# Kernel tuning notes

Hardware: AMD Instinct MI355X
Metric: run time of the kernel (lower is better)

The kernel has to match this reference:

```python
import jax, jax.numpy as jnp
import numpy as np

B, E, S, H = 8, 1024, 2048, 16  # batch, embed_dim, seq_len, n_heads
D = E // H                       # per-head hidden dim


def setup_inputs() -> dict:
    key = jax.random.key(0)
    k1, k2 = jax.random.split(key)
    x = jax.random.normal(k1, (B, E, S), dtype=jnp.float32)
    weight = jax.random.normal(k2, (H, S), dtype=jnp.float32)  # nn.Parameter(torch.randn)
    bias = jnp.zeros((H, S), dtype=jnp.float32)                # nn.Parameter(torch.zeros)
    return {"x": x, "weight": weight, "bias": bias}


def _vector_to_matrix(v):
    # v: (H, S) -> M: (H, S, S), M[h, i, j] = v[h, j - i] if j >= i else 0
    h, m = v.shape
    i = jnp.arange(m)[:, None]
    j = jnp.arange(m)[None, :]
    off = j - i  # negative offsets wrap (same as torch fancy indexing) but are masked out
    return jnp.where(j >= i, v[:, off], jnp.zeros((), dtype=v.dtype))


def reference(x, weight, bias):
    b, e, s = x.shape
    h = weight.shape[0]
    d = e // h
    M = _vector_to_matrix(weight)  # (H, S, S)
    # Original: x.view(B,H,D,S).reshape(B*H,D,S) paired with W.repeat_interleave(B,0),
    # i.e. flat index k uses M[k // B]. Group the flat B*H axis into H contiguous
    # blocks of size B so each block shares one Toeplitz matrix (no (B*H,S,S) blowup).
    xg = x.reshape(b * h, d, s).reshape(h, b, d, s)  # block m = M[m]
    out = jnp.einsum('mbds,mst->mbdt', xg, M) + bias[:, None, None, :]
    return out.reshape(b, e, s)
```

## Files before the change

### kernel.cpp

```cpp
#include <hip/hip_runtime.h>
#include <hip/hip_bf16.h>

#define SEQ    2048
#define NHEAD  16
#define RPH    512
#define BM     128
#define BK     64
#define NTH    512

#define WSTRIDE 2184
#define ABUF_E  8192
#define WCOP_E  (2 * ABUF_E)
#define TOT_E   (WCOP_E + 8 * WSTRIDE + 128)

typedef float  f32x4  __attribute__((ext_vector_type(4)));
typedef __bf16 bf16x8 __attribute__((ext_vector_type(8)));

struct PF { float4 v0, v1, v2, v3; };

__device__ __forceinline__ unsigned f2bf(float f) {
    union { __hip_bfloat16 h; unsigned short u; } cv;
    cv.h = __float2bfloat16(f);
    return (unsigned)cv.u;
}

__device__ __forceinline__ uint4 pack8u(float4 a, float4 b) {
    union { bf16x8 v; uint4 u; } r;
    r.v[0] = (__bf16)a.x; r.v[1] = (__bf16)a.y;
    r.v[2] = (__bf16)a.z; r.v[3] = (__bf16)a.w;
    r.v[4] = (__bf16)b.x; r.v[5] = (__bf16)b.y;
    r.v[6] = (__bf16)b.z; r.v[7] = (__bf16)b.w;
    return r.u;
}

#define MFMA16(a, b, c) __builtin_amdgcn_mfma_f32_16x16x32_bf16((a), (b), (c), 0, 0, 0)

#define LOADPF(P, CH)                                                         \
  { const float* g_ = Xp + (size_t)(CH) * BK;                                 \
    P.v0 = *(const float4*)g_;                                                \
    P.v1 = *(const float4*)(g_ + 4);                                          \
    P.v2 = *(const float4*)(g_ + 8);                                          \
    P.v3 = *(const float4*)(g_ + 12); }

#define WRITEA(AB, P)                                                         \
  { *(uint4*)((AB) + wb0) = pack8u(P.v0, P.v1);                               \
    *(uint4*)((AB) + wb1) = pack8u(P.v2, P.v3); }

#define WINLOAD4(CH, OFFE, S0, S1, S2, S3)                                    \
  { const unsigned short* bq_ = wcB + 64 * (CH) + (OFFE);                     \
    bw[S0] = *(const bf16x8*)(bq_);                                           \
    bw[S1] = *(const bf16x8*)(bq_ + 16);                                      \
    bw[S2] = *(const bf16x8*)(bq_ + 32);                                      \
    bw[S3] = *(const bf16x8*)(bq_ + 48); }

#define KSTEPW(ABC, KS, P8, BASE)                                             \
  { const int kb_ = (64 * (KS) + kq16) ^ swz;                                 \
    bf16x8 af0 = *(const bf16x8*)((ABC) + Arow0 + kb_);                       \
    bf16x8 af1 = *(const bf16x8*)((ABC) + Arow1 + kb_);                       \
    acc[0][0] = MFMA16(af0, bw[((P8)+(BASE)-0)&15], acc[0][0]);               \
    acc[1][0] = MFMA16(af1, bw[((P8)+(BASE)-0)&15], acc[1][0]);               \
    acc[0][1] = MFMA16(af0, bw[((P8)+(BASE)-1)&15], acc[0][1]);               \
    acc[1][1] = MFMA16(af1, bw[((P8)+(BASE)-1)&15], acc[1][1]);               \
    acc[0][2] = MFMA16(af0, bw[((P8)+(BASE)-2)&15], acc[0][2]);               \
    acc[1][2] = MFMA16(af1, bw[((P8)+(BASE)-2)&15], acc[1][2]);               \
    acc[0][3] = MFMA16(af0, bw[((P8)+(BASE)-3)&15], acc[0][3]);               \
    acc[1][3] = MFMA16(af1, bw[((P8)+(BASE)-3)&15], acc[1][3]);               \
    acc[0][4] = MFMA16(af0, bw[((P8)+(BASE)-4)&15], acc[0][4]);               \
    acc[1][4] = MFMA16(af1, bw[((P8)+(BASE)-4)&15], acc[1][4]);               \
    acc[0][5] = MFMA16(af0, bw[((P8)+(BASE)-5)&15], acc[0][5]);               \
    acc[1][5] = MFMA16(af1, bw[((P8)+(BASE)-5)&15], acc[1][5]);               \
    acc[0][6] = MFMA16(af0, bw[((P8)+(BASE)-6)&15], acc[0][6]);               \
    acc[1][6] = MFMA16(af1, bw[((P8)+(BASE)-6)&15], acc[1][6]);               \
    acc[0][7] = MFMA16(af0, bw[((P8)+(BASE)-7)&15], acc[0][7]);               \
    acc[1][7] = MFMA16(af1, bw[((P8)+(BASE)-7)&15], acc[1][7]); }

#define PAIRBODY(P8)                                                          \
  {                                                                           \
    WRITEA(ab1, pfB);                         \
    if (ch + 3 < nch) LOADPF(pfB, ch + 3);                                    \
    if (ch < nchw) {                                                          \
      __builtin_amdgcn_s_setprio(1);                                          \
      KSTEPW(ab0, 0, P8, 7);                                                  \
      KSTEPW(ab0, 1, P8, 9);                                                  \
      __builtin_amdgcn_s_setprio(0);                                          \
    }                                                                         \
    if (ch + 2 < nch)                                                         \
        WINLOAD4(ch, 112, ((P8)+14)&15, ((P8)+15)&15,                         \
                 ((P8)+16)&15, ((P8)+17)&15);                                 \
    asm volatile("s_waitcnt lgkmcnt(0)\n\ts_barrier" ::: "memory");           \
    if (ch + 2 < nch) WRITEA(ab0, pfA);       \
    if (ch + 4 < nch) LOADPF(pfA, ch + 4);                                    \
    if (ch + 1 < nchw) {                                                      \
      __builtin_amdgcn_s_setprio(1);                                          \
      KSTEPW(ab1, 0, P8, 11);                                                 \
      KSTEPW(ab1, 1, P8, 13);                                                 \
      __builtin_amdgcn_s_setprio(0);                                          \
    }                                                                         \
    if (ch + 2 < nch)                                                         \
        WINLOAD4(ch, 176, ((P8)+18)&15, ((P8)+19)&15,                         \
                 ((P8)+20)&15, ((P8)+21)&15);                                 \
    asm volatile("s_waitcnt lgkmcnt(0)\n\ts_barrier" ::: "memory");           \
  }

__global__ __launch_bounds__(NTH, 1) void mixer_kernel(
    const float* __restrict__ x, const float* __restrict__ wgt,
    const float* __restrict__ bias, float* __restrict__ out)
{
    __shared__ unsigned short smem[TOT_E] __attribute__((aligned(16)));
    char* ab0 = (char*)smem;
    char* ab1 = (char*)smem + ABUF_E * 2;
    unsigned short* wc = smem + WCOP_E;

    const int tid  = threadIdx.x;
    const int lane = tid & 63;
    const int wv   = tid >> 6;
    const int r    = wv & 3;
    const int tb   = wv >> 2;

    const int bid  = blockIdx.x;
    const int m    = (bid & 7) + 8 * ((bid >> 3) & 1);
    const int rt   = (bid >> 4) & 3;
    const int j    = 7 - (bid >> 6);
    const int nch  = 4 * j + 4;
    const int nchw = nch - 2 + 2 * tb;

    const float* Xb = x   + (size_t)(m * RPH + rt * BM) * SEQ;
    float*       Ob = out + (size_t)(m * RPH + rt * BM) * SEQ;
    const float* wr = wgt  + m * SEQ;
    const float* br = bias + m * SEQ;

    const int srow = 32 * r + 16 * tb + (lane >> 2);
    const int colq = lane & 3;
    const int wsw  = (srow & 7) << 4;
    const int wb0  = srow * 128 + ((colq * 32) ^ wsw);
    const int wb1  = srow * 128 + ((colq * 32 + 16) ^ wsw);
    const float* Xp = Xb + (size_t)srow * SEQ + colq * 16;

    PF pfA, pfB;
    LOADPF(pfA, 0);
    LOADPF(pfB, 1);

    if (tid < 256) {
        const int t8 = tid * 8;
        const float* g = wr + (2040 - t8);
        float4 lo = *(const float4*)g;
        float4 hi = *(const float4*)(g + 4);
        uint4 v;
        v.x = f2bf(hi.w) | (f2bf(hi.z) << 16);
        v.y = f2bf(hi.y) | (f2bf(hi.x) << 16);
        v.z = f2bf(lo.w) | (f2bf(lo.z) << 16);
        v.w = f2bf(lo.y) | (f2bf(lo.x) << 16);
        *(uint4*)(smem + 8 + t8) = v;
        if (tid < 21) {
            uint4 z = {0u, 0u, 0u, 0u};
            unsigned short* dst = (tid == 0) ? smem
                                 : smem + 8 + 2048 + (tid - 1) * 8;
            *(uint4*)dst = z;
        }
    }
    __syncthreads();

    #pragma unroll
    for (int c = 0; c < 8; ++c) {
        for (int grp = tid; grp < WSTRIDE / 8; grp += NTH) {
            const int i = grp * 8;
            uint4 g0 = *(const uint4*)(smem + 8 + i - 8);
            uint4 g1 = *(const uint4*)(smem + 8 + i);
            unsigned d[9] = {g0.x, g0.y, g0.z, g0.w,
                             g1.x, g1.y, g1.z, g1.w, 0u};
            const int qd = (16 - 2 * c) >> 2;
            uint4 o;
            if (c & 1) {
                o.x = (d[qd]     >> 16) | (d[qd + 1] << 16);
                o.y = (d[qd + 1] >> 16) | (d[qd + 2] << 16);
                o.z = (d[qd + 2] >> 16) | (d[qd + 3] << 16);
                o.w = (d[qd + 3] >> 16) | (d[qd + 4] << 16);
            } else {
                o.x = d[qd];     o.y = d[qd + 1];
                o.z = d[qd + 2]; o.w = d[qd + 3];
            }
            *(uint4*)(wc + c * WSTRIDE + i) = o;
        }
    }
    __syncthreads();

    const int col_low = lane & 15;
    const int kq      = lane >> 4;
    const int kq16    = kq * 16;
    const int swz     = (col_low & 7) << 4;
    const int rbw     = 32 * r;
    const int t0w     = 256 * j + 128 * tb;
    const int cpy     = (col_low + 1) & 7;
    const int BcBase  = cpy * WSTRIDE + cpy + 2047 - col_low + 8 * kq;
    const int Arow0   = (rbw      + col_low) * 128;
    const int Arow1   = (rbw + 16 + col_low) * 128;
    const unsigned short* wcB = wc + (BcBase - t0w);

    WRITEA(ab0, pfA);
    LOADPF(pfA, 2);

    bf16x8 bw[16];
    {
        const unsigned short* bq_ = wcB - 112;
        #pragma unroll
        for (int i = 0; i < 14; ++i)
            bw[i] = *(const bf16x8*)(bq_ + 16 * i);
    }
    __syncthreads();

    f32x4 acc[2][8] = {};
    int ch = 0;
    for (;;) {
        PAIRBODY(0);
        ch += 2; if (ch >= nch) break;
        PAIRBODY(8);
        ch += 2; if (ch >= nch) break;
    }

    #pragma unroll
    for (int c = 0; c < 8; ++c) {
        const int colg = t0w + 16 * c + col_low;
        const float bv = br[colg];
        #pragma unroll
        for (int a = 0; a < 2; ++a) {
            const int rowl = rbw + 16 * a + 4 * kq;
            #pragma unroll
            for (int rr = 0; rr < 4; ++rr)
                Ob[(size_t)(rowl + rr) * SEQ + colg] = acc[a][c][rr] + bv;
        }
    }
}

extern "C" void kernel_launch(void* const* d_in, const int* in_sizes, int n_in,
                              void* d_out, int out_size, void* d_ws, size_t ws_size,
                              hipStream_t stream) {
    const float* x  = (const float*)d_in[0];
    const float* w  = (const float*)d_in[1];
    const float* bs = (const float*)d_in[2];
    float* out = (float*)d_out;
    dim3 grid(512);
    dim3 block(NTH);
    hipLaunchKernelGGL(mixer_kernel, grid, block, 0, stream, x, w, bs, out);
}
```

Baseline: 44.70 us.

## Shrink register window and prefetch depth to allow higher occupancy

Replaces the 16-entry rotating B-fragment register window with an 8-entry window reloaded from LDS each chunk, and cuts the global prefetch buffers from two to one. Launch bounds rise from 1 to 4 blocks per CU so more waves can hide latency. The cost is extra LDS reads per chunk and a shallower global prefetch pipeline, which may expose memory latency if occupancy does not actually increase. LDS usage (about 67 KB per block) may still cap how many blocks fit per CU.

```diff
diff --git a/kernel.cpp b/kernel.cpp
--- a/kernel.cpp
+++ b/kernel.cpp
@@ -46,63 +46,73 @@
   { *(uint4*)((AB) + wb0) = pack8u(P.v0, P.v1);                               \
     *(uint4*)((AB) + wb1) = pack8u(P.v2, P.v3); }
 
-#define WINLOAD4(CH, OFFE, S0, S1, S2, S3)                                    \
-  { const unsigned short* bq_ = wcB + 64 * (CH) + (OFFE);                     \
-    bw[S0] = *(const bf16x8*)(bq_);                                           \
-    bw[S1] = *(const bf16x8*)(bq_ + 16);                                      \
-    bw[S2] = *(const bf16x8*)(bq_ + 32);                                      \
-    bw[S3] = *(const bf16x8*)(bq_ + 48); }
-
-#define KSTEPW(ABC, KS, P8, BASE)                                             \
-  { const int kb_ = (64 * (KS) + kq16) ^ swz;                                 \
+#define KSTEP0(ABC)                                                           \
+  { const int kb_ = kq16 ^ swz;                                               \
     bf16x8 af0 = *(const bf16x8*)((ABC) + Arow0 + kb_);                       \
     bf16x8 af1 = *(const bf16x8*)((ABC) + Arow1 + kb_);                       \
-    acc[0][0] = MFMA16(af0, bw[((P8)+(BASE)-0)&15], acc[0][0]);               \
-    acc[1][0] = MFMA16(af1, bw[((P8)+(BASE)-0)&15], acc[1][0]);               \
-    acc[0][1] = MFMA16(af0, bw[((P8)+(BASE)-1)&15], acc[0][1]);               \
-    acc[1][1] = MFMA16(af1, bw[((P8)+(BASE)-1)&15], acc[1][1]);               \
-    acc[0][2] = MFMA16(af0, bw[((P8)+(BASE)-2)&15], acc[0][2]);               \
-    acc[1][2] = MFMA16(af1, bw[((P8)+(BASE)-2)&15], acc[1][2]);               \
-    acc[0][3] = MFMA16(af0, bw[((P8)+(BASE)-3)&15], acc[0][3]);               \
-    acc[1][3] = MFMA16(af1, bw[((P8)+(BASE)-3)&15], acc[1][3]);               \
-    acc[0][4] = MFMA16(af0, bw[((P8)+(BASE)-4)&15], acc[0][4]);               \
-    acc[1][4] = MFMA16(af1, bw[((P8)+(BASE)-4)&15], acc[1][4]);               \
-    acc[0][5] = MFMA16(af0, bw[((P8)+(BASE)-5)&15], acc[0][5]);               \
-    acc[1][5] = MFMA16(af1, bw[((P8)+(BASE)-5)&15], acc[1][5]);               \
-    acc[0][6] = MFMA16(af0, bw[((P8)+(BASE)-6)&15], acc[0][6]);               \
-    acc[1][6] = MFMA16(af1, bw[((P8)+(BASE)-6)&15], acc[1][6]);               \
-    acc[0][7] = MFMA16(af0, bw[((P8)+(BASE)-7)&15], acc[0][7]);               \
-    acc[1][7] = MFMA16(af1, bw[((P8)+(BASE)-7)&15], acc[1][7]); }
-
-#define PAIRBODY(P8)                                                          \
+    acc[0][0] = MFMA16(af0, bw[7], acc[0][0]);                                \
+    acc[1][0] = MFMA16(af1, bw[7], acc[1][0]);                                \
+    acc[0][1] = MFMA16(af0, bw[6], acc[0][1]);                                \
+    acc[1][1] = MFMA16(af1, bw[6], acc[1][1]);                                \
+    acc[0][2] = MFMA16(af0, bw[5], acc[0][2]);                                \
+    acc[1][2] = MFMA16(af1, bw[5], acc[1][2]);                                \
+    acc[0][3] = MFMA16(af0, bw[4], acc[0][3]);                                \
+    acc[1][3] = MFMA16(af1, bw[4], acc[1][3]);                                \
+    acc[0][4] = MFMA16(af0, bw[3], acc[0][4]);                                \
+    acc[1][4] = MFMA16(af1, bw[3], acc[1][4]);                                \
+    acc[0][5] = MFMA16(af0, bw[2], acc[0][5]);                                \
+    acc[1][5] = MFMA16(af1, bw[2], acc[1][5]);                                \
+    acc[0][6] = MFMA16(af0, bw[1], acc[0][6]);                                \
+    acc[1][6] = MFMA16(af1, bw[1], acc[1][6]);                                \
+    acc[0][7] = MFMA16(af0, bw[0], acc[0][7]);                                \
+    acc[1][7] = MFMA16(af1, bw[0], acc[1][7]); }
+
+#define KSTEP1(ABC)                                                           \
+  { const int kb_ = (64 + kq16) ^ swz;                                        \
+    bf16x8 af0 = *(const bf16x8*)((ABC) + Arow0 + kb_);                       \
+    bf16x8 af1 = *(const bf16x8*)((ABC) + Arow1 + kb_);                       \
+    acc[0][7] = MFMA16(af0, bw[2], acc[0][7]);                                \
+    acc[1][7] = MFMA16(af1, bw[2], acc[1][7]);                                \
+    acc[0][6] = MFMA16(af0, bw[3], acc[0][6]);                                \
+    acc[1][6] = MFMA16(af1, bw[3], acc[1][6]);                                \
+    acc[0][5] = MFMA16(af0, bw[4], acc[0][5]);                                \
+    acc[1][5] = MFMA16(af1, bw[4], acc[1][5]);                                \
+    acc[0][4] = MFMA16(af0, bw[5], acc[0][4]);                                \
+    acc[1][4] = MFMA16(af1, bw[5], acc[1][4]);                                \
+    acc[0][3] = MFMA16(af0, bw[6], acc[0][3]);                                \
+    acc[1][3] = MFMA16(af1, bw[6], acc[1][3]);                                \
+    acc[0][2] = MFMA16(af0, bw[7], acc[0][2]);                                \
+    acc[1][2] = MFMA16(af1, bw[7], acc[1][2]);                                \
+    acc[0][1] = MFMA16(af0, bw[0], acc[0][1]);                                \
+    acc[1][1] = MFMA16(af1, bw[0], acc[1][1]);                                \
+    acc[0][0] = MFMA16(af0, bw[1], acc[0][0]);                                \
+    acc[1][0] = MFMA16(af1, bw[1], acc[1][0]); }
+
+#define CHUNKBODY(CH, ABC, ABN)                                               \
   {                                                                           \
-    WRITEA(ab1, pfB);                         \
-    if (ch + 3 < nch) LOADPF(pfB, ch + 3);                                    \
-    if (ch < nchw) {                                                          \
+    WRITEA(ABN, pf);                         \
+    if ((CH) + 2 < nch) LOADPF(pf, (CH) + 2);                                 \
+    if ((CH) < nchw) {                                                        \
+      const unsigned short* bq_ = wcB + 64 * (CH) - 112;                      \
+      bw[0] = *(const bf16x8*)(bq_);                                          \
+      bw[1] = *(const bf16x8*)(bq_ + 16);                                     \
+      bw[2] = *(const bf16x8*)(bq_ + 32);                                     \
+      bw[3] = *(const bf16x8*)(bq_ + 48);                                     \
+      bw[4] = *(const bf16x8*)(bq_ + 64);                                     \
+      bw[5] = *(const bf16x8*)(bq_ + 80);                                     \
+      bw[6] = *(const bf16x8*)(bq_ + 96);                                     \
+      bw[7] = *(const bf16x8*)(bq_ + 112);                                    \
       __builtin_amdgcn_s_setprio(1);                                          \
-      KSTEPW(ab0, 0, P8, 7);                                                  \
-      KSTEPW(ab0, 1, P8, 9);                                                  \
+      KSTEP0(ABC);                                                            \
+      bw[0] = *(const bf16x8*)(bq_ + 128);                        \
+      bw[1] = *(const bf16x8*)(bq_ + 144);                        \
+      KSTEP1(ABC);                                                            \
       __builtin_amdgcn_s_setprio(0);                                          \
     }                                                                         \
-    if (ch + 2 < nch)                                                         \
-        WINLOAD4(ch, 112, ((P8)+14)&15, ((P8)+15)&15,                         \
-                 ((P8)+16)&15, ((P8)+17)&15);                                 \
-    asm volatile("s_waitcnt lgkmcnt(0)\n\ts_barrier" ::: "memory");           \
-    if (ch + 2 < nch) WRITEA(ab0, pfA);       \
-    if (ch + 4 < nch) LOADPF(pfA, ch + 4);                                    \
-    if (ch + 1 < nchw) {                                                      \
-      __builtin_amdgcn_s_setprio(1);                                          \
-      KSTEPW(ab1, 0, P8, 11);                                                 \
-      KSTEPW(ab1, 1, P8, 13);                                                 \
-      __builtin_amdgcn_s_setprio(0);                                          \
-    }                                                                         \
-    if (ch + 2 < nch)                                                         \
-        WINLOAD4(ch, 176, ((P8)+18)&15, ((P8)+19)&15,                         \
-                 ((P8)+20)&15, ((P8)+21)&15);                                 \
     asm volatile("s_waitcnt lgkmcnt(0)\n\ts_barrier" ::: "memory");           \
   }
 
-__global__ __launch_bounds__(NTH, 1) void mixer_kernel(
+__global__ __launch_bounds__(NTH, 4) void mixer_kernel(
     const float* __restrict__ x, const float* __restrict__ wgt,
     const float* __restrict__ bias, float* __restrict__ out)
 {
@@ -136,9 +146,8 @@
     const int wb1  = srow * 128 + ((colq * 32 + 16) ^ wsw);
     const float* Xp = Xb + (size_t)srow * SEQ + colq * 16;
 
-    PF pfA, pfB;
-    LOADPF(pfA, 0);
-    LOADPF(pfB, 1);
+    PF pf;
+    LOADPF(pf, 0);
 
     if (tid < 256) {
         const int t8 = tid * 8;
@@ -196,25 +205,15 @@
     const int Arow1   = (rbw + 16 + col_low) * 128;
     const unsigned short* wcB = wc + (BcBase - t0w);
 
-    WRITEA(ab0, pfA);
-    LOADPF(pfA, 2);
-
-    bf16x8 bw[16];
-    {
-        const unsigned short* bq_ = wcB - 112;
-        #pragma unroll
-        for (int i = 0; i < 14; ++i)
-            bw[i] = *(const bf16x8*)(bq_ + 16 * i);
-    }
+    WRITEA(ab0, pf);
+    LOADPF(pf, 1);
     __syncthreads();
 
+    bf16x8 bw[8];
     f32x4 acc[2][8] = {};
-    int ch = 0;
-    for (;;) {
-        PAIRBODY(0);
-        ch += 2; if (ch >= nch) break;
-        PAIRBODY(8);
-        ch += 2; if (ch >= nch) break;
+    for (int ch = 0; ch < nch; ch += 2) {
+        CHUNKBODY(ch,     ab0, ab1);
+        CHUNKBODY(ch + 1, ab1, ab0);
     }
 
     #pragma unroll
```

New measurement: 43.95 us. Within noise of the previous version (-1.7%).
